# Optimization experiments

Measured on AMD Instinct MI355X. Metric: run time of the kernel, lower is better.

Reference implementation:

```python
import jax, jax.numpy as jnp
import numpy as np

N = 50000      # nodes
E = 800000     # edges
IN, HID, OUT, H = 128, 32, 128, 4
NEG_SLOPE = 0.2  # DGL GATConv default


def setup_inputs() -> dict:
    key = jax.random.key(0)
    ks = jax.random.split(key, 12)
    def w(k, shape, fan_in):
        return jax.random.normal(k, shape, dtype=jnp.float32) / np.sqrt(fan_in)
    return {
        "x": jax.random.normal(ks[0], (N, IN), dtype=jnp.float32),
        "src": jax.random.randint(ks[1], (E,), 0, N, dtype=jnp.int64),
        "dst": jax.random.randint(ks[2], (E,), 0, N, dtype=jnp.int64),
        # layer 0: GATConv(IN -> HID, H heads)
        "W0": w(ks[3], (IN, H * HID), IN),
        "attn_l0": w(ks[4], (H, HID), HID),
        "attn_r0": w(ks[5], (H, HID), HID),
        "bias0": jnp.zeros((H * HID,), dtype=jnp.float32),
        # layer 1: GATConv(H*HID -> OUT, 1 head)
        "W1": w(ks[6], (H * HID, OUT), H * HID),
        "attn_l1": w(ks[7], (1, OUT), OUT),
        "attn_r1": w(ks[8], (1, OUT), OUT),
        "bias1": jnp.zeros((OUT,), dtype=jnp.float32),
    }


def gat_conv(x, src, dst, W, attn_l, attn_r, bias, heads, feat_dim):
    """DGL GATConv: linear -> per-edge LeakyReLU attention -> edge softmax over
    destination neighborhoods -> weighted scatter-sum -> bias -> ELU."""
    n = x.shape[0]
    feat = (x @ W).reshape(n, heads, feat_dim)            # [N,H,F]
    el = jnp.einsum("nhf,hf->nh", feat, attn_l)           # [N,H]
    er = jnp.einsum("nhf,hf->nh", feat, attn_r)
    e = jax.nn.leaky_relu(el[src] + er[dst], NEG_SLOPE)    # [E,H]
    # segment softmax over incoming edges of each destination node
    e_max = jax.ops.segment_max(e, dst, num_segments=n)    # [N,H]
    exp_e = jnp.exp(e - e_max[dst])                        # [E,H]
    denom = jax.ops.segment_sum(exp_e, dst, num_segments=n)
    alpha = exp_e / denom[dst]                             # [E,H]
    msg = feat[src] * alpha[:, :, None]                    # [E,H,F]
    rst = jax.ops.segment_sum(msg, dst, num_segments=n)    # [N,H,F]
    rst = rst + bias.reshape(heads, feat_dim)
    return jax.nn.elu(rst)


def reference(x, src, dst, W0, attn_l0, attn_r0, bias0, W1, attn_l1, attn_r1, bias1):
    h = gat_conv(x, src, dst, W0, attn_l0, attn_r0, bias0, H, HID)   # [N,H,HID]
    h = h.reshape(h.shape[0], H * HID)                               # flatten(1)
    h = gat_conv(h, src, dst, W1, attn_l1, attn_r1, bias1, 1, OUT)   # [N,1,OUT]
    return h.mean(axis=1)                                            # [N,OUT]
```

## Files before the change

### kernel.cpp

```cpp
#include <hip/hip_runtime.h>

#define NEG_SLOPE 0.2f
#define NBMAX 256

typedef __attribute__((ext_vector_type(8))) short bf16x8;
typedef __attribute__((ext_vector_type(16))) float f32x16;

__device__ inline ushort bf16rne(float f) {
  uint u = __float_as_uint(f);
  u += 0x7fff + ((u >> 16) & 1);
  return (ushort)(u >> 16);
}
__device__ inline float bf2f(ushort h) { return __uint_as_float((uint)h << 16); }

#define XS(row, byte) ((byte) ^ (((row) & 15) << 4))

__global__ __launch_bounds__(256) void splitW(const float* __restrict__ W,
    ushort* __restrict__ Wh, ushort* __restrict__ Wl) {
  int i = blockIdx.x * 256 + threadIdx.x;
  int k = i >> 7, nn = i & 127;
  float w = W[i];
  ushort h = bf16rne(w);
  float lo = w - bf2f(h);
  Wh[nn * 128 + k] = h;
  Wl[nn * 128 + k] = bf16rne(lo);
}

__global__ __launch_bounds__(256) void gemm_mfma(const float* __restrict__ A,
    const ushort* __restrict__ Wh, const ushort* __restrict__ Wl,
    float* __restrict__ C, ushort* __restrict__ Cb, int n) {
  __shared__ __align__(16) ushort sAh[64 * 128];
  __shared__ __align__(16) ushort sAl[64 * 128];
  __shared__ __align__(16) ushort sBh[64 * 128];
  __shared__ __align__(16) ushort sBl[64 * 128];
  const int t = threadIdx.x;
  const int row0 = blockIdx.x * 64;
  const int col0 = blockIdx.y * 64;
  for (int i = t; i < 2048; i += 256) {
    int r = i >> 5, c4 = i & 31;
    int gr = row0 + r;
    float4 v = make_float4(0.f, 0.f, 0.f, 0.f);
    if (gr < n) v = ((const float4*)(A + (size_t)gr * 128))[c4];
    ushort4 h, l;
    h.x = bf16rne(v.x); l.x = bf16rne(v.x - bf2f(h.x));
    h.y = bf16rne(v.y); l.y = bf16rne(v.y - bf2f(h.y));
    h.z = bf16rne(v.z); l.z = bf16rne(v.z - bf2f(h.z));
    h.w = bf16rne(v.w); l.w = bf16rne(v.w - bf2f(h.w));
    int byte = XS(r, r * 256 + c4 * 8);
    *(ushort4*)((char*)sAh + byte) = h;
    *(ushort4*)((char*)sAl + byte) = l;
  }
  for (int i = t; i < 1024; i += 256) {
    int r = i >> 4, q = i & 15;
    int byte = XS(r, r * 256 + q * 16);
    *(uint4*)((char*)sBh + byte) = ((const uint4*)(Wh + (size_t)(col0 + r) * 128))[q];
    *(uint4*)((char*)sBl + byte) = ((const uint4*)(Wl + (size_t)(col0 + r) * 128))[q];
  }
  __syncthreads();
  const int w = t >> 6, lane = t & 63;
  const int rbase = (w >> 1) * 32;
  const int cbase = (w & 1) * 32;
  const int lr = lane & 31;
  const int hi = lane >> 5;
  const int arow = rbase + lr;
  const int brow = cbase + lr;
  f32x16 acc0 = {};
  f32x16 acc1 = {};
#pragma unroll
  for (int ks = 0; ks < 8; ++ks) {
    int kb = (ks * 16 + hi * 8) * 2;
    bf16x8 ah = *(bf16x8*)((char*)sAh + XS(arow, arow * 256 + kb));
    bf16x8 al = *(bf16x8*)((char*)sAl + XS(arow, arow * 256 + kb));
    bf16x8 bh = *(bf16x8*)((char*)sBh + XS(brow, brow * 256 + kb));
    bf16x8 bl = *(bf16x8*)((char*)sBl + XS(brow, brow * 256 + kb));
    if (ks & 1) {
      acc1 = __builtin_amdgcn_mfma_f32_32x32x16_bf16(ah, bh, acc1, 0, 0, 0);
      acc1 = __builtin_amdgcn_mfma_f32_32x32x16_bf16(ah, bl, acc1, 0, 0, 0);
      acc1 = __builtin_amdgcn_mfma_f32_32x32x16_bf16(al, bh, acc1, 0, 0, 0);
    } else {
      acc0 = __builtin_amdgcn_mfma_f32_32x32x16_bf16(ah, bh, acc0, 0, 0, 0);
      acc0 = __builtin_amdgcn_mfma_f32_32x32x16_bf16(ah, bl, acc0, 0, 0, 0);
      acc0 = __builtin_amdgcn_mfma_f32_32x32x16_bf16(al, bh, acc0, 0, 0, 0);
    }
  }
  const int gcol = col0 + cbase + lr;
#pragma unroll
  for (int r = 0; r < 16; ++r) {
    int grow = row0 + rbase + (r & 3) + 8 * (r >> 2) + 4 * hi;
    if (grow < n) {
      float v = acc0[r] + acc1[r];
      C[(size_t)grow * 128 + gcol] = v;
      Cb[(size_t)grow * 128 + gcol] = bf16rne(v);
    }
  }
}

__global__ __launch_bounds__(256) void node_attn4(const float* __restrict__ feat,
    const float* __restrict__ attn_l, const float* __restrict__ attn_r,
    float* __restrict__ el, float* __restrict__ er, int n4) {
  int i = blockIdx.x * 256 + threadIdx.x;
  if (i >= n4) return;
  const int h = i & 3;
  const float* f = feat + (size_t)i * 32;
  const float* al = attn_l + h * 32;
  const float* ar = attn_r + h * 32;
  float sl = 0.f, sr = 0.f;
#pragma unroll
  for (int k = 0; k < 32; k += 4) {
    float4 v = *(const float4*)(f + k);
    float4 a = *(const float4*)(al + k);
    float4 b = *(const float4*)(ar + k);
    sl += v.x * a.x + v.y * a.y + v.z * a.z + v.w * a.w;
    sr += v.x * b.x + v.y * b.y + v.z * b.z + v.w * b.w;
  }
  el[i] = sl;
  er[i] = sr;
}

__global__ __launch_bounds__(256) void node_attn1(const float* __restrict__ feat,
    const float* __restrict__ attn_l, const float* __restrict__ attn_r,
    float* __restrict__ el, float* __restrict__ er, int n) {
  int i = blockIdx.x * 256 + threadIdx.x;
  if (i >= n) return;
  const float* f = feat + (size_t)i * 128;
  float sl = 0.f, sr = 0.f;
#pragma unroll 8
  for (int k = 0; k < 128; k += 4) {
    float4 v = *(const float4*)(f + k);
    float4 a = *(const float4*)(attn_l + k);
    float4 b = *(const float4*)(attn_r + k);
    sl += v.x * a.x + v.y * a.y + v.z * a.z + v.w * a.w;
    sr += v.x * b.x + v.y * b.y + v.z * b.z + v.w * b.w;
  }
  el[i] = sl;
  er[i] = sr;
}

__global__ __launch_bounds__(1024) void bucket_count(const int* __restrict__ dst,
    int* __restrict__ bucketCount, int E_) {
  __shared__ int h[NBMAX];
  const int t = threadIdx.x;
  if (t < NBMAX) h[t] = 0;
  __syncthreads();
  const int base = blockIdx.x * 4096;
#pragma unroll
  for (int k = 0; k < 4; ++k) {
    int i = base + k * 1024 + t;
    if (i < E_) atomicAdd(&h[dst[i] >> 8], 1);
  }
  __syncthreads();
  if (t < NBMAX && h[t]) atomicAdd(&bucketCount[t], h[t]);
}

__global__ __launch_bounds__(256) void bucket_scan(const int* __restrict__ bucketCount,
    int* __restrict__ bucketOff, int* __restrict__ bucketCursor,
    int* __restrict__ rowptr, int nb, int n, int E_) {
  __shared__ int s[256];
  const int t = threadIdx.x;
  int v = (t < nb) ? bucketCount[t] : 0;
  s[t] = v;
  __syncthreads();
  for (int off = 1; off < 256; off <<= 1) {
    int u = (t >= off) ? s[t - off] : 0;
    __syncthreads();
    s[t] += u;
    __syncthreads();
  }
  int excl = s[t] - v;
  if (t < nb) { bucketOff[t] = excl; bucketCursor[t] = excl; }
  if (t == nb - 1) { bucketOff[nb] = s[t]; rowptr[n] = E_; }
}

__global__ __launch_bounds__(1024) void bucket_scatter(const int* __restrict__ src,
    const int* __restrict__ dst, int* __restrict__ bucketCursor,
    uint* __restrict__ bucketData, int E_) {
  __shared__ int h[NBMAX];
  __shared__ int bse[NBMAX];
  const int t = threadIdx.x;
  if (t < NBMAX) h[t] = 0;
  __syncthreads();
  const int base = blockIdx.x * 4096;
  int sv[4], dv[4], bk[4];
  bool ok[4];
#pragma unroll
  for (int k = 0; k < 4; ++k) {
    int i = base + k * 1024 + t;
    ok[k] = i < E_;
    if (ok[k]) {
      sv[k] = src[i];
      dv[k] = dst[i];
      bk[k] = dv[k] >> 8;
      atomicAdd(&h[bk[k]], 1);
    }
  }
  __syncthreads();
  if (t < NBMAX) {
    int c = h[t];
    bse[t] = c ? atomicAdd(&bucketCursor[t], c) : 0;
    h[t] = 0;
  }
  __syncthreads();
#pragma unroll
  for (int k = 0; k < 4; ++k) {
    if (ok[k]) {
      int r = atomicAdd(&h[bk[k]], 1);
      bucketData[bse[bk[k]] + r] = (uint)sv[k] | ((uint)(dv[k] & 255) << 16);
    }
  }
}

__global__ __launch_bounds__(1024) void fine_csr(const uint* __restrict__ bucketData,
    const int* __restrict__ bucketOff, int* __restrict__ rowptr,
    int* __restrict__ csr_src, int n) {
  __shared__ int fh[256];
  __shared__ int fx[256];
  const int b = blockIdx.x;
  const int t = threadIdx.x;
  const int beg = bucketOff[b];
  const int cnt = bucketOff[b + 1] - beg;
  if (t < 256) fh[t] = 0;
  __syncthreads();
  for (int i = t; i < cnt; i += 1024) atomicAdd(&fh[bucketData[beg + i] >> 16], 1);
  __syncthreads();
  if (t < 256) fx[t] = fh[t];
  __syncthreads();
  for (int off = 1; off < 256; off <<= 1) {
    int u = 0;
    if (t < 256 && t >= off) u = fx[t - off];
    __syncthreads();
    if (t < 256) fx[t] += u;
    __syncthreads();
  }
  if (t < 256) {
    int excl = fx[t] - fh[t];
    int node = b * 256 + t;
    if (node < n) rowptr[node] = beg + excl;
    fh[t] = excl;
  }
  __syncthreads();
  for (int i = t; i < cnt; i += 1024) {
    uint rec = bucketData[beg + i];
    int r = atomicAdd(&fh[rec >> 16], 1);
    csr_src[beg + r] = (int)(rec & 0xffffu);
  }
}

__global__ __launch_bounds__(256) void aggregate4(const int* __restrict__ rowptr,
    const int* __restrict__ csr_src, const ushort* __restrict__ featb,
    const float* __restrict__ el, const float* __restrict__ er,
    const float* __restrict__ bias, float* __restrict__ out, int n) {
  int node = blockIdx.x * 4 + (threadIdx.x >> 6);
  if (node >= n) return;
  const int lane = threadIdx.x & 63;
  const int f0 = lane * 2;
  const int h = lane >> 4;
  const float erh = er[(size_t)node * 4 + h];
  float a0 = 0.f, a1 = 0.f, d = 0.f;
  const int beg = rowptr[node], end = rowptr[node + 1];
  int idx = beg;
  for (; idx + 3 < end; idx += 4) {
    int s0 = csr_src[idx + 0];
    int s1 = csr_src[idx + 1];
    int s2 = csr_src[idx + 2];
    int s3 = csr_src[idx + 3];
    float l0 = el[(size_t)s0 * 4 + h];
    float l1 = el[(size_t)s1 * 4 + h];
    float l2 = el[(size_t)s2 * 4 + h];
    float l3 = el[(size_t)s3 * 4 + h];
    uint v0 = *(const uint*)(featb + (size_t)s0 * 128 + f0);
    uint v1 = *(const uint*)(featb + (size_t)s1 * 128 + f0);
    uint v2 = *(const uint*)(featb + (size_t)s2 * 128 + f0);
    uint v3 = *(const uint*)(featb + (size_t)s3 * 128 + f0);
    float e0 = l0 + erh; e0 = e0 > 0.f ? e0 : NEG_SLOPE * e0; float w0 = __expf(e0);
    float e1 = l1 + erh; e1 = e1 > 0.f ? e1 : NEG_SLOPE * e1; float w1 = __expf(e1);
    float e2 = l2 + erh; e2 = e2 > 0.f ? e2 : NEG_SLOPE * e2; float w2 = __expf(e2);
    float e3 = l3 + erh; e3 = e3 > 0.f ? e3 : NEG_SLOPE * e3; float w3 = __expf(e3);
    a0 += __uint_as_float(v0 << 16) * w0; a1 += __uint_as_float(v0 & 0xffff0000u) * w0;
    a0 += __uint_as_float(v1 << 16) * w1; a1 += __uint_as_float(v1 & 0xffff0000u) * w1;
    a0 += __uint_as_float(v2 << 16) * w2; a1 += __uint_as_float(v2 & 0xffff0000u) * w2;
    a0 += __uint_as_float(v3 << 16) * w3; a1 += __uint_as_float(v3 & 0xffff0000u) * w3;
    d += w0 + w1 + w2 + w3;
  }
  for (; idx < end; ++idx) {
    int s = csr_src[idx];
    float e = el[(size_t)s * 4 + h] + erh;
    e = e > 0.f ? e : NEG_SLOPE * e;
    float w = __expf(e);
    uint v = *(const uint*)(featb + (size_t)s * 128 + f0);
    a0 += __uint_as_float(v << 16) * w;
    a1 += __uint_as_float(v & 0xffff0000u) * w;
    d += w;
  }
  float inv = d > 0.f ? 1.f / d : 0.f;
  float v0 = a0 * inv + bias[f0];
  v0 = v0 > 0.f ? v0 : __expf(v0) - 1.f;
  float v1 = a1 * inv + bias[f0 + 1];
  v1 = v1 > 0.f ? v1 : __expf(v1) - 1.f;
  *(float2*)(out + (size_t)node * 128 + f0) = make_float2(v0, v1);
}

__global__ __launch_bounds__(256) void aggregate1(const int* __restrict__ rowptr,
    const int* __restrict__ csr_src, const ushort* __restrict__ featb,
    const float* __restrict__ el, const float* __restrict__ er,
    const float* __restrict__ bias, float* __restrict__ out, int n) {
  int node = blockIdx.x * 4 + (threadIdx.x >> 6);
  if (node >= n) return;
  const int lane = threadIdx.x & 63;
  const int f0 = lane * 2;
  const float erv = er[node];
  float a0 = 0.f, a1 = 0.f, d = 0.f;
  const int beg = rowptr[node], end = rowptr[node + 1];
  int idx = beg;
  for (; idx + 3 < end; idx += 4) {
    int s0 = csr_src[idx + 0];
    int s1 = csr_src[idx + 1];
    int s2 = csr_src[idx + 2];
    int s3 = csr_src[idx + 3];
    float l0 = el[s0];
    float l1 = el[s1];
    float l2 = el[s2];
    float l3 = el[s3];
    uint v0 = *(const uint*)(featb + (size_t)s0 * 128 + f0);
    uint v1 = *(const uint*)(featb + (size_t)s1 * 128 + f0);
    uint v2 = *(const uint*)(featb + (size_t)s2 * 128 + f0);
    uint v3 = *(const uint*)(featb + (size_t)s3 * 128 + f0);
    float e0 = l0 + erv; e0 = e0 > 0.f ? e0 : NEG_SLOPE * e0; float w0 = __expf(e0);
    float e1 = l1 + erv; e1 = e1 > 0.f ? e1 : NEG_SLOPE * e1; float w1 = __expf(e1);
    float e2 = l2 + erv; e2 = e2 > 0.f ? e2 : NEG_SLOPE * e2; float w2 = __expf(e2);
    float e3 = l3 + erv; e3 = e3 > 0.f ? e3 : NEG_SLOPE * e3; float w3 = __expf(e3);
    a0 += __uint_as_float(v0 << 16) * w0; a1 += __uint_as_float(v0 & 0xffff0000u) * w0;
    a0 += __uint_as_float(v1 << 16) * w1; a1 += __uint_as_float(v1 & 0xffff0000u) * w1;
    a0 += __uint_as_float(v2 << 16) * w2; a1 += __uint_as_float(v2 & 0xffff0000u) * w2;
    a0 += __uint_as_float(v3 << 16) * w3; a1 += __uint_as_float(v3 & 0xffff0000u) * w3;
    d += w0 + w1 + w2 + w3;
  }
  for (; idx < end; ++idx) {
    int s = csr_src[idx];
    float e = el[s] + erv;
    e = e > 0.f ? e : NEG_SLOPE * e;
    float w = __expf(e);
    uint v = *(const uint*)(featb + (size_t)s * 128 + f0);
    a0 += __uint_as_float(v << 16) * w;
    a1 += __uint_as_float(v & 0xffff0000u) * w;
    d += w;
  }
  float inv = d > 0.f ? 1.f / d : 0.f;
  float v0 = a0 * inv + bias[f0];
  v0 = v0 > 0.f ? v0 : __expf(v0) - 1.f;
  float v1 = a1 * inv + bias[f0 + 1];
  v1 = v1 > 0.f ? v1 : __expf(v1) - 1.f;
  *(float2*)(out + (size_t)node * 128 + f0) = make_float2(v0, v1);
}

extern "C" void kernel_launch(void* const* d_in, const int* in_sizes, int n_in,
                              void* d_out, int out_size, void* d_ws, size_t ws_size,
                              hipStream_t stream) {
  const float* x   = (const float*)d_in[0];
  const int*   src = (const int*)d_in[1];
  const int*   dst = (const int*)d_in[2];
  const float* W0  = (const float*)d_in[3];
  const float* al0 = (const float*)d_in[4];
  const float* ar0 = (const float*)d_in[5];
  const float* b0  = (const float*)d_in[6];
  const float* W1  = (const float*)d_in[7];
  const float* al1 = (const float*)d_in[8];
  const float* ar1 = (const float*)d_in[9];
  const float* b1  = (const float*)d_in[10];
  float* out = (float*)d_out;
  const int n  = in_sizes[0] / 128;
  const int E_ = in_sizes[1];

  char* p = (char*)d_ws;
  auto alloc = [&](size_t bytes) {
    char* r = p;
    p += (bytes + 255) & ~(size_t)255;
    return r;
  };
  float*  feat0  = (float*)alloc((size_t)n * 128 * 4);
  ushort* feat0b = (ushort*)alloc((size_t)n * 128 * 2);
  float*  h0     = (float*)alloc((size_t)n * 128 * 4);
  float*  feat1  = (float*)alloc((size_t)n * 128 * 4);
  ushort* feat1b = (ushort*)alloc((size_t)n * 128 * 2);
  float* el0   = (float*)alloc((size_t)n * 4 * 4);
  float* er0   = (float*)alloc((size_t)n * 4 * 4);
  float* el1   = (float*)alloc((size_t)n * 4);
  float* er1   = (float*)alloc((size_t)n * 4);
  int* rowptr  = (int*)alloc((size_t)(n + 1) * 4);
  int* csr_src = (int*)alloc((size_t)E_ * 4);
  uint* bucketData  = (uint*)alloc((size_t)E_ * 4);
  int* bucketCount  = (int*)alloc(NBMAX * 4);
  int* bucketOff    = (int*)alloc((NBMAX + 1) * 4);
  int* bucketCursor = (int*)alloc(NBMAX * 4);
  ushort* W0h = (ushort*)alloc(128 * 128 * 2);
  ushort* W0l = (ushort*)alloc(128 * 128 * 2);
  ushort* W1h = (ushort*)alloc(128 * 128 * 2);
  ushort* W1l = (ushort*)alloc(128 * 128 * 2);

  const int nbk = (n + 255) >> 8;
  const int gb  = (E_ + 4095) / 4096;

  hipMemsetAsync(bucketCount, 0, NBMAX * 4, stream);

  splitW<<<64, 256, 0, stream>>>(W0, W0h, W0l);
  splitW<<<64, 256, 0, stream>>>(W1, W1h, W1l);

  bucket_count<<<gb, 1024, 0, stream>>>(dst, bucketCount, E_);
  bucket_scan<<<1, 256, 0, stream>>>(bucketCount, bucketOff, bucketCursor, rowptr, nbk, n, E_);
  bucket_scatter<<<gb, 1024, 0, stream>>>(src, dst, bucketCursor, bucketData, E_);
  fine_csr<<<nbk, 1024, 0, stream>>>(bucketData, bucketOff, rowptr, csr_src, n);

  dim3 gg((n + 63) / 64, 2);

  gemm_mfma<<<gg, 256, 0, stream>>>(x, W0h, W0l, feat0, feat0b, n);
  node_attn4<<<(n * 4 + 255) / 256, 256, 0, stream>>>(feat0, al0, ar0, el0, er0, n * 4);
  aggregate4<<<(n + 3) / 4, 256, 0, stream>>>(rowptr, csr_src, feat0b, el0, er0, b0, h0, n);

  gemm_mfma<<<gg, 256, 0, stream>>>(h0, W1h, W1l, feat1, feat1b, n);
  node_attn1<<<(n + 255) / 256, 256, 0, stream>>>(feat1, al1, ar1, el1, er1, n);
  aggregate1<<<(n + 3) / 4, 256, 0, stream>>>(rowptr, csr_src, feat1b, el1, er1, b1, out, n);
}
```

Baseline: 196.5 us.

## Precompute per-edge attention weights in a separate edge kernel before aggregation

Packs the destination node into the CSR records, so each entry holds source (low 16 bits) and destination (high 16 bits). A new per-edge kernel computes exp(leaky_relu(el+er)) once per edge, for all heads, and writes the weights to a buffer reused from feat0/feat1. Aggregation kernels then read the precomputed weight instead of gathering el and recomputing the exponential in every lane. Before, each of the 16 lanes per head repeated that exp, and aggregate1's 64 lanes all repeated it. The cost is an extra launch and an extra E×4 float buffer written then read. The 16-bit packing limits node ids to below 65536.

New measurement: 204.9 us. 1.04x slower.

```diff
diff --git a/kernel.cpp b/kernel.cpp
--- a/kernel.cpp
+++ b/kernel.cpp
@@ -211,7 +211,7 @@
 
 __global__ __launch_bounds__(1024) void fine_csr(const uint* __restrict__ bucketData,
     const int* __restrict__ bucketOff, int* __restrict__ rowptr,
-    int* __restrict__ csr_src, int n) {
+    uint* __restrict__ csr, int n) {
   __shared__ int fh[256];
   __shared__ int fx[256];
   const int b = blockIdx.x;
@@ -238,43 +238,68 @@
     fh[t] = excl;
   }
   __syncthreads();
+  const uint nodeBase = (uint)b << 8;
   for (int i = t; i < cnt; i += 1024) {
     uint rec = bucketData[beg + i];
     int r = atomicAdd(&fh[rec >> 16], 1);
-    csr_src[beg + r] = (int)(rec & 0xffffu);
-  }
+    csr[beg + r] = (rec & 0xffffu) | ((nodeBase + (rec >> 16)) << 16);
+  }
+}
+
+__global__ __launch_bounds__(256) void edge_w4(const uint* __restrict__ csr,
+    const float* __restrict__ el, const float* __restrict__ er,
+    float* __restrict__ w4, int E_) {
+  int i = blockIdx.x * 256 + threadIdx.x;
+  if (i >= E_) return;
+  uint rec = csr[i];
+  int s = rec & 0xffffu, d = rec >> 16;
+  float4 l = ((const float4*)el)[s];
+  float4 r = ((const float4*)er)[d];
+  float e;
+  float4 w;
+  e = l.x + r.x; e = e > 0.f ? e : NEG_SLOPE * e; w.x = __expf(e);
+  e = l.y + r.y; e = e > 0.f ? e : NEG_SLOPE * e; w.y = __expf(e);
+  e = l.z + r.z; e = e > 0.f ? e : NEG_SLOPE * e; w.z = __expf(e);
+  e = l.w + r.w; e = e > 0.f ? e : NEG_SLOPE * e; w.w = __expf(e);
+  ((float4*)w4)[i] = w;
+}
+
+__global__ __launch_bounds__(256) void edge_w1(const uint* __restrict__ csr,
+    const float* __restrict__ el, const float* __restrict__ er,
+    float* __restrict__ w1, int E_) {
+  int i = blockIdx.x * 256 + threadIdx.x;
+  if (i >= E_) return;
+  uint rec = csr[i];
+  float e = el[rec & 0xffffu] + er[rec >> 16];
+  e = e > 0.f ? e : NEG_SLOPE * e;
+  w1[i] = __expf(e);
 }
 
 __global__ __launch_bounds__(256) void aggregate4(const int* __restrict__ rowptr,
-    const int* __restrict__ csr_src, const ushort* __restrict__ featb,
-    const float* __restrict__ el, const float* __restrict__ er,
-    const float* __restrict__ bias, float* __restrict__ out, int n) {
+    const uint* __restrict__ csr, const ushort* __restrict__ featb,
+    const float* __restrict__ w4f, const float* __restrict__ bias,
+    float* __restrict__ out, int n) {
   int node = blockIdx.x * 4 + (threadIdx.x >> 6);
   if (node >= n) return;
   const int lane = threadIdx.x & 63;
   const int f0 = lane * 2;
   const int h = lane >> 4;
-  const float erh = er[(size_t)node * 4 + h];
   float a0 = 0.f, a1 = 0.f, d = 0.f;
   const int beg = rowptr[node], end = rowptr[node + 1];
   int idx = beg;
   for (; idx + 3 < end; idx += 4) {
-    int s0 = csr_src[idx + 0];
-    int s1 = csr_src[idx + 1];
-    int s2 = csr_src[idx + 2];
-    int s3 = csr_src[idx + 3];
-    float l0 = el[(size_t)s0 * 4 + h];
-    float l1 = el[(size_t)s1 * 4 + h];
-    float l2 = el[(size_t)s2 * 4 + h];
-    float l3 = el[(size_t)s3 * 4 + h];
-    uint v0 = *(const uint*)(featb + (size_t)s0 * 128 + f0);
-    uint v1 = *(const uint*)(featb + (size_t)s1 * 128 + f0);
-    uint v2 = *(const uint*)(featb + (size_t)s2 * 128 + f0);
-    uint v3 = *(const uint*)(featb + (size_t)s3 * 128 + f0);
-    float e0 = l0 + erh; e0 = e0 > 0.f ? e0 : NEG_SLOPE * e0; float w0 = __expf(e0);
-    float e1 = l1 + erh; e1 = e1 > 0.f ? e1 : NEG_SLOPE * e1; float w1 = __expf(e1);
-    float e2 = l2 + erh; e2 = e2 > 0.f ? e2 : NEG_SLOPE * e2; float w2 = __expf(e2);
-    float e3 = l3 + erh; e3 = e3 > 0.f ? e3 : NEG_SLOPE * e3; float w3 = __expf(e3);
+    uint r0 = csr[idx + 0];
+    uint r1 = csr[idx + 1];
+    uint r2 = csr[idx + 2];
+    uint r3 = csr[idx + 3];
+    float w0 = w4f[(idx + 0) * 4 + h];
+    float w1 = w4f[(idx + 1) * 4 + h];
+    float w2 = w4f[(idx + 2) * 4 + h];
+    float w3 = w4f[(idx + 3) * 4 + h];
+    uint v0 = *(const uint*)(featb + (size_t)(r0 & 0xffffu) * 128 + f0);
+    uint v1 = *(const uint*)(featb + (size_t)(r1 & 0xffffu) * 128 + f0);
+    uint v2 = *(const uint*)(featb + (size_t)(r2 & 0xffffu) * 128 + f0);
+    uint v3 = *(const uint*)(featb + (size_t)(r3 & 0xffffu) * 128 + f0);
     a0 += __uint_as_float(v0 << 16) * w0; a1 += __uint_as_float(v0 & 0xffff0000u) * w0;
     a0 += __uint_as_float(v1 << 16) * w1; a1 += __uint_as_float(v1 & 0xffff0000u) * w1;
     a0 += __uint_as_float(v2 << 16) * w2; a1 += __uint_as_float(v2 & 0xffff0000u) * w2;
@@ -282,11 +307,9 @@
     d += w0 + w1 + w2 + w3;
   }
   for (; idx < end; ++idx) {
-    int s = csr_src[idx];
-    float e = el[(size_t)s * 4 + h] + erh;
-    e = e > 0.f ? e : NEG_SLOPE * e;
-    float w = __expf(e);
-    uint v = *(const uint*)(featb + (size_t)s * 128 + f0);
+    uint r = csr[idx];
+    float w = w4f[idx * 4 + h];
+    uint v = *(const uint*)(featb + (size_t)(r & 0xffffu) * 128 + f0);
     a0 += __uint_as_float(v << 16) * w;
     a1 += __uint_as_float(v & 0xffff0000u) * w;
     d += w;
@@ -300,34 +323,29 @@
 }
 
 __global__ __launch_bounds__(256) void aggregate1(const int* __restrict__ rowptr,
-    const int* __restrict__ csr_src, const ushort* __restrict__ featb,
-    const float* __restrict__ el, const float* __restrict__ er,
-    const float* __restrict__ bias, float* __restrict__ out, int n) {
+    const uint* __restrict__ csr, const ushort* __restrict__ featb,
+    const float* __restrict__ w1f, const float* __restrict__ bias,
+    float* __restrict__ out, int n) {
   int node = blockIdx.x * 4 + (threadIdx.x >> 6);
   if (node >= n) return;
   const int lane = threadIdx.x & 63;
   const int f0 = lane * 2;
-  const float erv = er[node];
   float a0 = 0.f, a1 = 0.f, d = 0.f;
   const int beg = rowptr[node], end = rowptr[node + 1];
   int idx = beg;
   for (; idx + 3 < end; idx += 4) {
-    int s0 = csr_src[idx + 0];
-    int s1 = csr_src[idx + 1];
-    int s2 = csr_src[idx + 2];
-    int s3 = csr_src[idx + 3];
-    float l0 = el[s0];
-    float l1 = el[s1];
-    float l2 = el[s2];
-    float l3 = el[s3];
-    uint v0 = *(const uint*)(featb + (size_t)s0 * 128 + f0);
-    uint v1 = *(const uint*)(featb + (size_t)s1 * 128 + f0);
-    uint v2 = *(const uint*)(featb + (size_t)s2 * 128 + f0);
-    uint v3 = *(const uint*)(featb + (size_t)s3 * 128 + f0);
-    float e0 = l0 + erv; e0 = e0 > 0.f ? e0 : NEG_SLOPE * e0; float w0 = __expf(e0);
-    float e1 = l1 + erv; e1 = e1 > 0.f ? e1 : NEG_SLOPE * e1; float w1 = __expf(e1);
-    float e2 = l2 + erv; e2 = e2 > 0.f ? e2 : NEG_SLOPE * e2; float w2 = __expf(e2);
-    float e3 = l3 + erv; e3 = e3 > 0.f ? e3 : NEG_SLOPE * e3; float w3 = __expf(e3);
+    uint r0 = csr[idx + 0];
+    uint r1 = csr[idx + 1];
+    uint r2 = csr[idx + 2];
+    uint r3 = csr[idx + 3];
+    float w0 = w1f[idx + 0];
+    float w1 = w1f[idx + 1];
+    float w2 = w1f[idx + 2];
+    float w3 = w1f[idx + 3];
+    uint v0 = *(const uint*)(featb + (size_t)(r0 & 0xffffu) * 128 + f0);
+    uint v1 = *(const uint*)(featb + (size_t)(r1 & 0xffffu) * 128 + f0);
+    uint v2 = *(const uint*)(featb + (size_t)(r2 & 0xffffu) * 128 + f0);
+    uint v3 = *(const uint*)(featb + (size_t)(r3 & 0xffffu) * 128 + f0);
     a0 += __uint_as_float(v0 << 16) * w0; a1 += __uint_as_float(v0 & 0xffff0000u) * w0;
     a0 += __uint_as_float(v1 << 16) * w1; a1 += __uint_as_float(v1 & 0xffff0000u) * w1;
     a0 += __uint_as_float(v2 << 16) * w2; a1 += __uint_as_float(v2 & 0xffff0000u) * w2;
@@ -335,11 +353,9 @@
     d += w0 + w1 + w2 + w3;
   }
   for (; idx < end; ++idx) {
-    int s = csr_src[idx];
-    float e = el[s] + erv;
-    e = e > 0.f ? e : NEG_SLOPE * e;
-    float w = __expf(e);
-    uint v = *(const uint*)(featb + (size_t)s * 128 + f0);
+    uint r = csr[idx];
+    float w = w1f[idx];
+    uint v = *(const uint*)(featb + (size_t)(r & 0xffffu) * 128 + f0);
     a0 += __uint_as_float(v << 16) * w;
     a1 += __uint_as_float(v & 0xffff0000u) * w;
     d += w;
@@ -386,7 +402,7 @@
   float* el1   = (float*)alloc((size_t)n * 4);
   float* er1   = (float*)alloc((size_t)n * 4);
   int* rowptr  = (int*)alloc((size_t)(n + 1) * 4);
-  int* csr_src = (int*)alloc((size_t)E_ * 4);
+  uint* csr    = (uint*)alloc((size_t)E_ * 4);
   uint* bucketData  = (uint*)alloc((size_t)E_ * 4);
   int* bucketCount  = (int*)alloc(NBMAX * 4);
   int* bucketOff    = (int*)alloc((NBMAX + 1) * 4);
@@ -395,9 +411,12 @@
   ushort* W0l = (ushort*)alloc(128 * 128 * 2);
   ushort* W1h = (ushort*)alloc(128 * 128 * 2);
   ushort* W1l = (ushort*)alloc(128 * 128 * 2);
+  float* w4 = feat1;
+  float* w1 = feat0;
 
   const int nbk = (n + 255) >> 8;
   const int gb  = (E_ + 4095) / 4096;
+  const int eb  = (E_ + 255) / 256;
 
   hipMemsetAsync(bucketCount, 0, NBMAX * 4, stream);
 
@@ -407,15 +426,17 @@
   bucket_count<<<gb, 1024, 0, stream>>>(dst, bucketCount, E_);
   bucket_scan<<<1, 256, 0, stream>>>(bucketCount, bucketOff, bucketCursor, rowptr, nbk, n, E_);
   bucket_scatter<<<gb, 1024, 0, stream>>>(src, dst, bucketCursor, bucketData, E_);
-  fine_csr<<<nbk, 1024, 0, stream>>>(bucketData, bucketOff, rowptr, csr_src, n);
+  fine_csr<<<nbk, 1024, 0, stream>>>(bucketData, bucketOff, rowptr, csr, n);
 
   dim3 gg((n + 63) / 64, 2);
 
   gemm_mfma<<<gg, 256, 0, stream>>>(x, W0h, W0l, feat0, feat0b, n);
   node_attn4<<<(n * 4 + 255) / 256, 256, 0, stream>>>(feat0, al0, ar0, el0, er0, n * 4);
-  aggregate4<<<(n + 3) / 4, 256, 0, stream>>>(rowptr, csr_src, feat0b, el0, er0, b0, h0, n);
+  edge_w4<<<eb, 256, 0, stream>>>(csr, el0, er0, w4, E_);
+  aggregate4<<<(n + 3) / 4, 256, 0, stream>>>(rowptr, csr, feat0b, w4, b0, h0, n);
 
   gemm_mfma<<<gg, 256, 0, stream>>>(h0, W1h, W1l, feat1, feat1b, n);
   node_attn1<<<(n + 255) / 256, 256, 0, stream>>>(feat1, al1, ar1, el1, er1, n);
-  aggregate1<<<(n + 3) / 4, 256, 0, stream>>>(rowptr, csr_src, feat1b, el1, er1, b1, out, n);
-}
+  edge_w1<<<eb, 256, 0, stream>>>(csr, el1, er1, w1, E_);
+  aggregate1<<<(n + 3) / 4, 256, 0, stream>>>(rowptr, csr, feat1b, w1, b1, out, n);
+}
```
